# Kernel optimization log

Measured on AMD Instinct MI355X. Metric: run time of the kernel, lower is better.

The kernel has to match this reference:

```python
import jax, jax.numpy as jnp
import numpy as np

V = 30522   # bert-base-uncased vocab size
B, S, D, J, K = 2, 512, 768, 12, 4
NUM_LABELS = 7


def setup_inputs() -> dict:
    key = jax.random.key(0)
    ks = jax.random.split(key, 9)
    return {
        "sequence_output": jax.random.normal(ks[0], (B, S, D), jnp.float32),
        "input_ids": jax.random.randint(ks[1], (B, S), 0, V),
        "neighbors": jax.random.randint(ks[2], (B, S, J, K), 0, V),
        "W_mlp": jax.random.normal(ks[3], (J * D, 13 * D), jnp.float32) * 0.02,
        "b_mlp": jnp.zeros((J * D,), jnp.float32),
        "W_attn": jax.random.normal(ks[4], (D, 2 * D), jnp.float32) * 0.02,
        "b_attn": jnp.zeros((D,), jnp.float32),
        "W_cls": jax.random.normal(ks[5], (NUM_LABELS, 2 * D), jnp.float32) * 0.02,
        "b_cls": jnp.zeros((NUM_LABELS,), jnp.float32),
    }


def _gather_neighbors(sequence_output, input_ids, neighbors):
    """Replicates the dict-based gather-sum. The torch dict persists ACROSS
    batch elements (it is never reset), with later positions overwriting
    earlier ones (last occurrence wins). We carry a [V,D] table + presence
    mask through a scan over the batch dim."""
    pos = jnp.arange(S, dtype=jnp.int32)

    def step(carry, xs):
        table, present = carry            # [V,D], [V] bool
        ids, seq, nb = xs                 # [S], [S,D], [S,J,K]
        # last occurrence index of each vocab id in this example (-1 if absent)
        last_idx = jnp.full((V,), -1, jnp.int32).at[ids].max(pos)
        found = last_idx >= 0
        table = jnp.where(found[:, None],
                          seq[jnp.clip(last_idx, 0, S - 1)], table)
        present = present | found
        # sum neighbor embeddings that are present in the dictionary
        emb = jnp.where(present[nb][..., None], table[nb], 0.0).sum(axis=2)  # [S,J,D]
        return (table, present), emb

    init = (jnp.zeros((V, D), sequence_output.dtype), jnp.zeros((V,), bool))
    _, fn = jax.lax.scan(step, init, (input_ids, sequence_output, neighbors))
    return fn                              # [B,S,J,D]


def reference(sequence_output, input_ids, neighbors,
              W_mlp, b_mlp, W_attn, b_attn, W_cls, b_cls):
    fn = _gather_neighbors(sequence_output, input_ids, neighbors)  # [B,S,J,D]
    n_flat = fn.reshape(B, S, J * D)
    # gated MLP: rij = [row ; neighbors], g = sigmoid(W rij), c' = g * n
    rij = jnp.concatenate([sequence_output, n_flat], axis=-1)      # [B,S,13D]
    g = jax.nn.sigmoid(jnp.einsum('bsf,gf->bsg', rij, W_mlp) + b_mlp)
    c = (g * n_flat).reshape(B, S, J, D)                           # [B,S,J,D]
    # Luong-style attention: query = token embedding, context = gated neighbors
    scores = jnp.einsum('bsd,bsjd->bsj', sequence_output, c)
    attn = jax.nn.softmax(scores, axis=-1)
    mix = jnp.einsum('bsj,bsjd->bsd', attn, c)                     # [B,S,D]
    combined = jnp.concatenate([mix, sequence_output], axis=-1)    # [B,S,2D]
    attn_out = jnp.tanh(jnp.einsum('bsf,df->bsd', combined, W_attn) + b_attn)
    final = jnp.concatenate([sequence_output, attn_out], axis=-1)  # [B,S,2D]
    # dropout is identity at inference
    logits = jnp.einsum('bsf,lf->bsl', final, W_cls) + b_cls       # [B,S,7]
    return logits
```

## Files before the change

kernel.cpp:

```cpp
#include <hip/hip_runtime.h>
#include <hip/hip_bf16.h>

#define V_PAD  30528
#define S_LEN  512
#define D_DIM  768
#define J_N    12
#define M_ROWS 1024
#define K_MLP  9984
#define N_MLP  9216
#define K_ATT  1536
#define N_ATT  768
#define N_LBL  7

using bf16x8 = __attribute__((ext_vector_type(8))) __bf16;
using f32x4  = __attribute__((ext_vector_type(4))) float;

__device__ __forceinline__ unsigned short f2bf(float f) {
  union { float f; unsigned int u; } c; c.f = f;
  unsigned int u = c.u;
  return (unsigned short)((u + 0x7fffu + ((u >> 16) & 1u)) >> 16);
}
__device__ __forceinline__ float bf2f(unsigned short h) {
  union { unsigned int u; float f; } c; c.u = (unsigned int)h << 16; return c.f;
}

__global__ __launch_bounds__(256)
void cvt_bf16_kernel(const float* __restrict__ in, unsigned short* __restrict__ out) {
  size_t i = (size_t)blockIdx.x * 256 + threadIdx.x;
  const float4 f0 = ((const float4*)in)[i * 2];
  const float4 f1 = ((const float4*)in)[i * 2 + 1];
  union { unsigned short h[8]; uint4 q; } pk;
  pk.h[0] = f2bf(f0.x); pk.h[1] = f2bf(f0.y); pk.h[2] = f2bf(f0.z); pk.h[3] = f2bf(f0.w);
  pk.h[4] = f2bf(f1.x); pk.h[5] = f2bf(f1.y); pk.h[6] = f2bf(f1.z); pk.h[7] = f2bf(f1.w);
  ((uint4*)out)[i] = pk.q;
}

__global__ void build_tables_kernel(const int* __restrict__ ids,
                                    int* __restrict__ last0,
                                    int* __restrict__ last01) {
  int p = blockIdx.x * 256 + threadIdx.x;
  if (p < M_ROWS) {
    int id = ids[p];
    atomicMax(&last01[id], p);
    if (p < S_LEN) atomicMax(&last0[id], p);
  }
}

__global__ __launch_bounds__(256) void seqrij_kernel(const float* __restrict__ seq,
                                                     unsigned short* __restrict__ rij) {
  int bs = blockIdx.x;
  for (int d = threadIdx.x; d < D_DIM; d += 256)
    rij[(size_t)bs * K_MLP + d] = f2bf(seq[(size_t)bs * D_DIM + d]);
}

template <bool WRITE_NFLAT>
__global__ __launch_bounds__(192)
void gather_kernel(const float* __restrict__ seq, const int* __restrict__ nbr,
                   const int* __restrict__ last0, const int* __restrict__ last01,
                   float* __restrict__ nflat, unsigned short* __restrict__ rij) {
  const int bsj = blockIdx.x;
  const int j  = bsj % J_N;
  const int bs = bsj / J_N;
  const int b  = bs >> 9;
  const int* nb = nbr + (size_t)bsj * 4;
  const int* tab = (b == 0) ? last0 : last01;
  const int s0 = tab[nb[0]], s1 = tab[nb[1]], s2 = tab[nb[2]], s3 = tab[nb[3]];
  const int d4 = threadIdx.x;
  float4 a = {0.f, 0.f, 0.f, 0.f};
  if (s0 >= 0) { float4 v = ((const float4*)(seq + (size_t)s0 * D_DIM))[d4]; a.x += v.x; a.y += v.y; a.z += v.z; a.w += v.w; }
  if (s1 >= 0) { float4 v = ((const float4*)(seq + (size_t)s1 * D_DIM))[d4]; a.x += v.x; a.y += v.y; a.z += v.z; a.w += v.w; }
  if (s2 >= 0) { float4 v = ((const float4*)(seq + (size_t)s2 * D_DIM))[d4]; a.x += v.x; a.y += v.y; a.z += v.z; a.w += v.w; }
  if (s3 >= 0) { float4 v = ((const float4*)(seq + (size_t)s3 * D_DIM))[d4]; a.x += v.x; a.y += v.y; a.z += v.z; a.w += v.w; }
  union { unsigned short h[4]; unsigned long long q; } pk;
  pk.h[0] = f2bf(a.x); pk.h[1] = f2bf(a.y); pk.h[2] = f2bf(a.z); pk.h[3] = f2bf(a.w);
  *(unsigned long long*)(rij + (size_t)bs * K_MLP + D_DIM + j * D_DIM + d4 * 4) = pk.q;
  if (WRITE_NFLAT)
    ((float4*)(nflat + (size_t)bs * N_MLP + j * D_DIM))[d4] = a;
}

template <int MODE, int TM, int TN, bool BF16B>
__global__ __launch_bounds__(256)
void gemm_nt_kernel(const unsigned short* __restrict__ A,
                    const void* __restrict__ Wv,
                    const float* __restrict__ bias,
                    float* __restrict__ nflat_c,
                    float* __restrict__ outp,
                    int K, int N, int kchunk) {
  constexpr int FM = TM / 32;
  constexpr int FN = TN / 32;
  __shared__ unsigned short ldsA[TM * 32];
  __shared__ unsigned short ldsB[TN * 32];
  const int tid  = threadIdx.x;
  const int lane = tid & 63;
  const int w    = tid >> 6;
  const int m0 = blockIdx.x * TM;
  const int n0 = blockIdx.y * TN;
  const int kb = blockIdx.z * kchunk;

  f32x4 acc[FM][FN];
#pragma unroll
  for (int i = 0; i < FM; ++i)
#pragma unroll
    for (int j = 0; j < FN; ++j) acc[i][j] = (f32x4){0.f, 0.f, 0.f, 0.f};

  const int lr = lane >> 2;
  const int lc = (lane & 3) * 8;
  const int wm = (w >> 1) * (TM / 2), wn = (w & 1) * (TN / 2);
  const int fr = lane & 15;
  const int fk = (lane >> 4) * 8;

  for (int kk = kb; kk < kb + kchunk; kk += 32) {
#pragma unroll
    for (int q = 0; q < TM / 64; ++q) {
      const int r = w * (TM / 4) + q * 16;
      const unsigned short* g = A + (size_t)(m0 + r + lr) * K + kk + lc;
      __builtin_amdgcn_global_load_lds(
          (const __attribute__((address_space(1))) void*)g,
          (__attribute__((address_space(3))) void*)(&ldsA[r * 32]), 16, 0, 0);
    }
    if (BF16B) {
#pragma unroll
      for (int q = 0; q < TN / 64; ++q) {
        const int r = w * (TN / 4) + q * 16;
        const unsigned short* g = (const unsigned short*)Wv +
                                  (size_t)(n0 + r + lr) * K + kk + lc;
        __builtin_amdgcn_global_load_lds(
            (const __attribute__((address_space(1))) void*)g,
            (__attribute__((address_space(3))) void*)(&ldsB[r * 32]), 16, 0, 0);
      }
    } else {
      constexpr int EPT = TN / 8;
      constexpr int TPR = 32 / EPT;
      const int br = tid / TPR, bc = (tid % TPR) * EPT;
      const float* g = (const float*)Wv + (size_t)(n0 + br) * K + kk + bc;
      union { unsigned short h[EPT]; uint4 q[EPT / 8]; } pk;
#pragma unroll
      for (int e = 0; e < EPT; e += 4) {
        float4 f = *(const float4*)(g + e);
        pk.h[e] = f2bf(f.x); pk.h[e + 1] = f2bf(f.y);
        pk.h[e + 2] = f2bf(f.z); pk.h[e + 3] = f2bf(f.w);
      }
      uint4* dst = (uint4*)&ldsB[br * 32 + bc];
#pragma unroll
      for (int e = 0; e < EPT / 8; ++e) dst[e] = pk.q[e];
    }
    __syncthreads();
    bf16x8 aF[FM], bF[FN];
#pragma unroll
    for (int i = 0; i < FM; ++i) aF[i] = *(const bf16x8*)&ldsA[(wm + i * 16 + fr) * 32 + fk];
#pragma unroll
    for (int j = 0; j < FN; ++j) bF[j] = *(const bf16x8*)&ldsB[(wn + j * 16 + fr) * 32 + fk];
#pragma unroll
    for (int i = 0; i < FM; ++i)
#pragma unroll
      for (int j = 0; j < FN; ++j)
        acc[i][j] = __builtin_amdgcn_mfma_f32_16x16x32_bf16(aF[i], bF[j], acc[i][j], 0, 0, 0);
    __syncthreads();
  }

  const size_t zoff = (MODE == 2) ? (size_t)blockIdx.z * M_ROWS * N : 0;
#pragma unroll
  for (int i = 0; i < FM; ++i) {
    int gm0 = m0 + wm + i * 16 + (lane >> 4) * 4;
#pragma unroll
    for (int j = 0; j < FN; ++j) {
      int gn = n0 + wn + j * 16 + (lane & 15);
      float bv = (MODE == 2) ? 0.f : bias[gn];
#pragma unroll
      for (int r = 0; r < 4; ++r) {
        size_t idx = (size_t)(gm0 + r) * N + gn;
        float x = acc[i][j][r] + bv;
        if (MODE == 0) {
          float gg = 1.0f / (1.0f + __expf(-x));
          nflat_c[idx] = gg * nflat_c[idx];
        } else if (MODE == 1) {
          outp[idx] = tanhf(x);
        } else {
          outp[zoff + idx] = x;
        }
      }
    }
  }
}

__global__ __launch_bounds__(256)
void attn_fused_kernel(const float* __restrict__ seq,
                       const float* __restrict__ p0, const float* __restrict__ p1,
                       const float* __restrict__ bmlp,
                       const unsigned short* __restrict__ rij,
                       unsigned short* __restrict__ combined) {
  __shared__ float sc[N_MLP];
  __shared__ float sq[D_DIM];
  __shared__ float ss[J_N];
  const int m = blockIdx.x;
  const int tid = threadIdx.x, lane = tid & 63, w = tid >> 6;
  for (int d = tid; d < D_DIM; d += 256) sq[d] = seq[(size_t)m * D_DIM + d];
  const float* q0 = p0 + (size_t)m * N_MLP;
  const float* q1 = p1 + (size_t)m * N_MLP;
  const unsigned short* nrow = rij + (size_t)m * K_MLP + D_DIM;
  for (int d = tid; d < N_MLP; d += 256) {
    float z = q0[d] + q1[d] + bmlp[d];
    float g = 1.0f / (1.0f + __expf(-z));
    sc[d] = g * bf2f(nrow[d]);
  }
  __syncthreads();
#pragma unroll
  for (int jj = 0; jj < 3; ++jj) {
    int j = w * 3 + jj;
    float p = 0.f;
    for (int d = lane; d < D_DIM; d += 64) p += sq[d] * sc[j * D_DIM + d];
#pragma unroll
    for (int off = 32; off > 0; off >>= 1) p += __shfl_down(p, off);
    if (lane == 0) ss[j] = p;
  }
  __syncthreads();
  float mx = ss[0];
#pragma unroll
  for (int j = 1; j < J_N; ++j) mx = fmaxf(mx, ss[j]);
  float aw[J_N]; float sum = 0.f;
#pragma unroll
  for (int j = 0; j < J_N; ++j) { aw[j] = __expf(ss[j] - mx); sum += aw[j]; }
  float inv = 1.f / sum;
  for (int d = tid; d < D_DIM; d += 256) {
    float mix = 0.f;
#pragma unroll
    for (int j = 0; j < J_N; ++j) mix += aw[j] * sc[j * D_DIM + d];
    combined[(size_t)m * K_ATT + d]         = f2bf(mix * inv);
    combined[(size_t)m * K_ATT + D_DIM + d] = f2bf(sq[d]);
  }
}

__global__ __launch_bounds__(256)
void attn_kernel(const float* __restrict__ seq, const float* __restrict__ c,
                 unsigned short* __restrict__ combined) {
  __shared__ float sc[N_MLP];
  __shared__ float sq[D_DIM];
  __shared__ float ss[J_N];
  const int m = blockIdx.x;
  const int tid = threadIdx.x, lane = tid & 63, w = tid >> 6;
  const float* crow = c + (size_t)m * N_MLP;
  for (int d = tid; d < N_MLP; d += 256) sc[d] = crow[d];
  for (int d = tid; d < D_DIM; d += 256) sq[d] = seq[(size_t)m * D_DIM + d];
  __syncthreads();
#pragma unroll
  for (int jj = 0; jj < 3; ++jj) {
    int j = w * 3 + jj;
    float p = 0.f;
    for (int d = lane; d < D_DIM; d += 64) p += sq[d] * sc[j * D_DIM + d];
#pragma unroll
    for (int off = 32; off > 0; off >>= 1) p += __shfl_down(p, off);
    if (lane == 0) ss[j] = p;
  }
  __syncthreads();
  float mx = ss[0];
#pragma unroll
  for (int j = 1; j < J_N; ++j) mx = fmaxf(mx, ss[j]);
  float aw[J_N]; float sum = 0.f;
#pragma unroll
  for (int j = 0; j < J_N; ++j) { aw[j] = __expf(ss[j] - mx); sum += aw[j]; }
  float inv = 1.f / sum;
  for (int d = tid; d < D_DIM; d += 256) {
    float mix = 0.f;
#pragma unroll
    for (int j = 0; j < J_N; ++j) mix += aw[j] * sc[j * D_DIM + d];
    combined[(size_t)m * K_ATT + d]         = f2bf(mix * inv);
    combined[(size_t)m * K_ATT + D_DIM + d] = f2bf(sq[d]);
  }
}

__global__ __launch_bounds__(256)
void cls_kernel(const float* __restrict__ seq, const float* __restrict__ attnout,
                const float* __restrict__ Wc, const float* __restrict__ bc,
                float* __restrict__ out) {
  __shared__ float part[4][N_LBL];
  const int m = blockIdx.x, tid = threadIdx.x, lane = tid & 63, w = tid >> 6;
  float p[N_LBL] = {0.f, 0.f, 0.f, 0.f, 0.f, 0.f, 0.f};
  for (int f = tid; f < K_ATT; f += 256) {
    float v = (f < D_DIM) ? seq[(size_t)m * D_DIM + f]
                          : attnout[(size_t)m * D_DIM + (f - D_DIM)];
#pragma unroll
    for (int l = 0; l < N_LBL; ++l) p[l] += v * Wc[l * K_ATT + f];
  }
#pragma unroll
  for (int l = 0; l < N_LBL; ++l) {
#pragma unroll
    for (int off = 32; off > 0; off >>= 1) p[l] += __shfl_down(p[l], off);
  }
  if (lane == 0) {
#pragma unroll
    for (int l = 0; l < N_LBL; ++l) part[w][l] = p[l];
  }
  __syncthreads();
  if (tid < N_LBL)
    out[(size_t)m * N_LBL + tid] =
        part[0][tid] + part[1][tid] + part[2][tid] + part[3][tid] + bc[tid];
}

extern "C" void kernel_launch(void* const* d_in, const int* in_sizes, int n_in,
                              void* d_out, int out_size, void* d_ws, size_t ws_size,
                              hipStream_t stream) {
  const float* seq   = (const float*)d_in[0];
  const int*   ids   = (const int*)d_in[1];
  const int*   nbr   = (const int*)d_in[2];
  const float* Wmlp  = (const float*)d_in[3];
  const float* bmlp  = (const float*)d_in[4];
  const float* Wattn = (const float*)d_in[5];
  const float* battn = (const float*)d_in[6];
  const float* Wcls  = (const float*)d_in[7];
  const float* bcls  = (const float*)d_in[8];
  float* out = (float*)d_out;

  char* ws = (char*)d_ws;
  size_t off = 0;
  int* last0  = (int*)(ws + off); off += (size_t)V_PAD * 4;
  int* last01 = (int*)(ws + off); off += (size_t)V_PAD * 4;
  unsigned short* rij = (unsigned short*)(ws + off); off += (size_t)M_ROWS * K_MLP * 2;
  unsigned short* combined = (unsigned short*)(ws + off); off += (size_t)M_ROWS * K_ATT * 2;
  float* attnout = (float*)(ws + off); off += (size_t)M_ROWS * N_ATT * 4;
  const size_t common = off;

  size_t ob = common;
  unsigned short* Wb_mlp  = (unsigned short*)(ws + ob); ob += (size_t)N_MLP * K_MLP * 2;
  unsigned short* Wb_attn = (unsigned short*)(ws + ob); ob += (size_t)N_ATT * K_ATT * 2;
  float* p0 = (float*)(ws + ob); ob += (size_t)M_ROWS * N_MLP * 4;
  float* p1 = (float*)(ws + ob); ob += (size_t)M_ROWS * N_MLP * 4;
  size_t om = common;
  float* nflat_m = (float*)(ws + om); om += (size_t)M_ROWS * N_MLP * 4;
  unsigned short* Wm_mlp  = (unsigned short*)(ws + om); om += (size_t)N_MLP * K_MLP * 2;
  unsigned short* Wm_attn = (unsigned short*)(ws + om); om += (size_t)N_ATT * K_ATT * 2;
  size_t os = common + (size_t)M_ROWS * N_MLP * 4;

  hipMemsetAsync(last0, 0xFF, (size_t)2 * V_PAD * 4, stream);
  build_tables_kernel<<<(M_ROWS + 255) / 256, 256, 0, stream>>>(ids, last0, last01);
  seqrij_kernel<<<M_ROWS, 256, 0, stream>>>(seq, rij);

  if (ws_size >= ob) {
    gather_kernel<false><<<M_ROWS * J_N, 192, 0, stream>>>(seq, nbr, last0, last01, nullptr, rij);
    cvt_bf16_kernel<<<(N_MLP * K_MLP) / (256 * 8), 256, 0, stream>>>(Wmlp, Wb_mlp);
    cvt_bf16_kernel<<<(N_ATT * K_ATT) / (256 * 8), 256, 0, stream>>>(Wattn, Wb_attn);
    gemm_nt_kernel<2, 128, 128, true><<<dim3(M_ROWS / 128, N_MLP / 128, 2), 256, 0, stream>>>(
        rij, Wb_mlp, nullptr, nullptr, p0, K_MLP, N_MLP, K_MLP / 2);
    attn_fused_kernel<<<M_ROWS, 256, 0, stream>>>(seq, p0, p1, bmlp, rij, combined);
    gemm_nt_kernel<1, 64, 64, true><<<dim3(M_ROWS / 64, N_ATT / 64), 256, 0, stream>>>(
        combined, Wb_attn, battn, nullptr, attnout, K_ATT, N_ATT, K_ATT);
  } else if (ws_size >= om) {
    gather_kernel<true><<<M_ROWS * J_N, 192, 0, stream>>>(seq, nbr, last0, last01, nflat_m, rij);
    cvt_bf16_kernel<<<(N_MLP * K_MLP) / (256 * 8), 256, 0, stream>>>(Wmlp, Wm_mlp);
    cvt_bf16_kernel<<<(N_ATT * K_ATT) / (256 * 8), 256, 0, stream>>>(Wattn, Wm_attn);
    gemm_nt_kernel<0, 128, 64, true><<<dim3(M_ROWS / 128, N_MLP / 64), 256, 0, stream>>>(
        rij, Wm_mlp, bmlp, nflat_m, nullptr, K_MLP, N_MLP, K_MLP);
    attn_kernel<<<M_ROWS, 256, 0, stream>>>(seq, nflat_m, combined);
    gemm_nt_kernel<1, 64, 64, true><<<dim3(M_ROWS / 64, N_ATT / 64), 256, 0, stream>>>(
        combined, Wm_attn, battn, nullptr, attnout, K_ATT, N_ATT, K_ATT);
  } else {
    float* nflat_s = nflat_m;
    (void)os;
    gather_kernel<true><<<M_ROWS * J_N, 192, 0, stream>>>(seq, nbr, last0, last01, nflat_s, rij);
    gemm_nt_kernel<0, 128, 64, false><<<dim3(M_ROWS / 128, N_MLP / 64), 256, 0, stream>>>(
        rij, Wmlp, bmlp, nflat_s, nullptr, K_MLP, N_MLP, K_MLP);
    attn_kernel<<<M_ROWS, 256, 0, stream>>>(seq, nflat_s, combined);
    gemm_nt_kernel<1, 64, 64, false><<<dim3(M_ROWS / 64, N_ATT / 64), 256, 0, stream>>>(
        combined, Wattn, battn, nullptr, attnout, K_ATT, N_ATT, K_ATT);
  }
  cls_kernel<<<M_ROWS, 256, 0, stream>>>(seq, attnout, Wcls, bcls, out);
}
```

Measured before the change: 899.7 us.

## Double-buffer GEMM LDS tiles, XOR-swizzle LDS layout, and remap blocks per XCD

The GEMM kernel now uses two LDS buffers, so the next K-slice is staged while MFMAs run on the current one, which also removes one barrier per iteration. LDS columns are XOR-swizzled on both write and read to reduce bank conflicts on the fragment loads. Large GEMMs also remap block IDs so that blocks sharing a weight tile land on the same XCD, aiming for better L2 reuse. In exchange, LDS use doubles, which may lower occupancy for the 128x128 tile, and the swizzle math must match on both the load and read sides.

Measured after the change: 861.0 us. 4.3% less time.

```diff
diff --git a/kernel.cpp b/kernel.cpp
--- a/kernel.cpp
+++ b/kernel.cpp
@@ -78,7 +78,7 @@
     ((float4*)(nflat + (size_t)bs * N_MLP + j * D_DIM))[d4] = a;
 }
 
-template <int MODE, int TM, int TN, bool BF16B>
+template <int MODE, int TM, int TN, bool BF16B, bool SWZ>
 __global__ __launch_bounds__(256)
 void gemm_nt_kernel(const unsigned short* __restrict__ A,
                     const void* __restrict__ Wv,
@@ -88,14 +88,26 @@
                     int K, int N, int kchunk) {
   constexpr int FM = TM / 32;
   constexpr int FN = TN / 32;
-  __shared__ unsigned short ldsA[TM * 32];
-  __shared__ unsigned short ldsB[TN * 32];
+  __shared__ unsigned short ldsA[2][TM * 32];
+  __shared__ unsigned short ldsB[2][TN * 32];
   const int tid  = threadIdx.x;
   const int lane = tid & 63;
   const int w    = tid >> 6;
-  const int m0 = blockIdx.x * TM;
-  const int n0 = blockIdx.y * TN;
-  const int kb = blockIdx.z * kchunk;
+
+  int bx = blockIdx.x, by = blockIdx.y, bz = blockIdx.z;
+  if (SWZ) {
+    const unsigned l   = blockIdx.x + gridDim.x * (blockIdx.y + gridDim.y * blockIdx.z);
+    const unsigned xcd = l & 7u;
+    const unsigned c   = l >> 3;
+    const unsigned gpx = (gridDim.y * gridDim.z) >> 3;
+    const unsigned g   = xcd * gpx + c / gridDim.x;
+    bx = (int)(c % gridDim.x);
+    by = (int)(g % gridDim.y);
+    bz = (int)(g / gridDim.y);
+  }
+  const int m0 = bx * TM;
+  const int n0 = by * TN;
+  const int kb = bz * kchunk;
 
   f32x4 acc[FM][FN];
 #pragma unroll
@@ -103,62 +115,73 @@
 #pragma unroll
     for (int j = 0; j < FN; ++j) acc[i][j] = (f32x4){0.f, 0.f, 0.f, 0.f};
 
-  const int lr = lane >> 2;
-  const int lc = (lane & 3) * 8;
+  const int lr  = lane >> 2;
+  const int lcs = (((lane & 3) ^ ((lane >> 3) & 3)) * 8);
   const int wm = (w >> 1) * (TM / 2), wn = (w & 1) * (TN / 2);
-  const int fr = lane & 15;
-  const int fk = (lane >> 4) * 8;
-
-  for (int kk = kb; kk < kb + kchunk; kk += 32) {
+  const int fr  = lane & 15;
+  const int fc  = (((lane >> 4) ^ ((fr >> 1) & 3)) * 8);
+
+  auto stage = [&](int buf, int kk) {
 #pragma unroll
     for (int q = 0; q < TM / 64; ++q) {
       const int r = w * (TM / 4) + q * 16;
-      const unsigned short* g = A + (size_t)(m0 + r + lr) * K + kk + lc;
+      const unsigned short* gsrc = A + (size_t)(m0 + r + lr) * K + kk + lcs;
       __builtin_amdgcn_global_load_lds(
-          (const __attribute__((address_space(1))) void*)g,
-          (__attribute__((address_space(3))) void*)(&ldsA[r * 32]), 16, 0, 0);
+          (const __attribute__((address_space(1))) void*)gsrc,
+          (__attribute__((address_space(3))) void*)(&ldsA[buf][r * 32]), 16, 0, 0);
     }
     if (BF16B) {
 #pragma unroll
       for (int q = 0; q < TN / 64; ++q) {
         const int r = w * (TN / 4) + q * 16;
-        const unsigned short* g = (const unsigned short*)Wv +
-                                  (size_t)(n0 + r + lr) * K + kk + lc;
+        const unsigned short* gsrc = (const unsigned short*)Wv +
+                                     (size_t)(n0 + r + lr) * K + kk + lcs;
         __builtin_amdgcn_global_load_lds(
-            (const __attribute__((address_space(1))) void*)g,
-            (__attribute__((address_space(3))) void*)(&ldsB[r * 32]), 16, 0, 0);
+            (const __attribute__((address_space(1))) void*)gsrc,
+            (__attribute__((address_space(3))) void*)(&ldsB[buf][r * 32]), 16, 0, 0);
       }
     } else {
       constexpr int EPT = TN / 8;
       constexpr int TPR = 32 / EPT;
       const int br = tid / TPR, bc = (tid % TPR) * EPT;
-      const float* g = (const float*)Wv + (size_t)(n0 + br) * K + kk + bc;
-      union { unsigned short h[EPT]; uint4 q[EPT / 8]; } pk;
-#pragma unroll
-      for (int e = 0; e < EPT; e += 4) {
-        float4 f = *(const float4*)(g + e);
-        pk.h[e] = f2bf(f.x); pk.h[e + 1] = f2bf(f.y);
-        pk.h[e + 2] = f2bf(f.z); pk.h[e + 3] = f2bf(f.w);
+      const float* gsrc = (const float*)Wv + (size_t)(n0 + br) * K + kk + bc;
+      const int brs = (br >> 1) & 3;
+#pragma unroll
+      for (int e = 0; e < EPT; e += 8) {
+        union { unsigned short h[8]; uint4 q4; } pk;
+#pragma unroll
+        for (int e2 = 0; e2 < 8; e2 += 4) {
+          float4 f = *(const float4*)(gsrc + e + e2);
+          pk.h[e2]     = f2bf(f.x); pk.h[e2 + 1] = f2bf(f.y);
+          pk.h[e2 + 2] = f2bf(f.z); pk.h[e2 + 3] = f2bf(f.w);
+        }
+        const int slot = ((bc + e) >> 3) ^ brs;
+        *(uint4*)&ldsB[buf][br * 32 + slot * 8] = pk.q4;
       }
-      uint4* dst = (uint4*)&ldsB[br * 32 + bc];
-#pragma unroll
-      for (int e = 0; e < EPT / 8; ++e) dst[e] = pk.q[e];
     }
+  };
+
+  const int nt = kchunk >> 5;
+  stage(0, kb);
+  for (int t = 0; t < nt; ++t) {
+    const int cur = t & 1;
     __syncthreads();
+    if (t + 1 < nt) stage(cur ^ 1, kb + (t + 1) * 32);
     bf16x8 aF[FM], bF[FN];
 #pragma unroll
-    for (int i = 0; i < FM; ++i) aF[i] = *(const bf16x8*)&ldsA[(wm + i * 16 + fr) * 32 + fk];
-#pragma unroll
-    for (int j = 0; j < FN; ++j) bF[j] = *(const bf16x8*)&ldsB[(wn + j * 16 + fr) * 32 + fk];
+    for (int i = 0; i < FM; ++i)
+      aF[i] = *(const bf16x8*)&ldsA[cur][(wm + i * 16 + fr) * 32 + fc];
+#pragma unroll
+    for (int j = 0; j < FN; ++j)
+      bF[j] = *(const bf16x8*)&ldsB[cur][(wn + j * 16 + fr) * 32 + fc];
 #pragma unroll
     for (int i = 0; i < FM; ++i)
 #pragma unroll
       for (int j = 0; j < FN; ++j)
         acc[i][j] = __builtin_amdgcn_mfma_f32_16x16x32_bf16(aF[i], bF[j], acc[i][j], 0, 0, 0);
-    __syncthreads();
-  }
-
-  const size_t zoff = (MODE == 2) ? (size_t)blockIdx.z * M_ROWS * N : 0;
+  }
+
+  const size_t zoff = (MODE == 2) ? (size_t)bz * M_ROWS * N : 0;
 #pragma unroll
   for (int i = 0; i < FM; ++i) {
     int gm0 = m0 + wm + i * 16 + (lane >> 4) * 4;
@@ -338,28 +361,28 @@
     gather_kernel<false><<<M_ROWS * J_N, 192, 0, stream>>>(seq, nbr, last0, last01, nullptr, rij);
     cvt_bf16_kernel<<<(N_MLP * K_MLP) / (256 * 8), 256, 0, stream>>>(Wmlp, Wb_mlp);
     cvt_bf16_kernel<<<(N_ATT * K_ATT) / (256 * 8), 256, 0, stream>>>(Wattn, Wb_attn);
-    gemm_nt_kernel<2, 128, 128, true><<<dim3(M_ROWS / 128, N_MLP / 128, 2), 256, 0, stream>>>(
+    gemm_nt_kernel<2, 128, 128, true, true><<<dim3(M_ROWS / 128, N_MLP / 128, 2), 256, 0, stream>>>(
         rij, Wb_mlp, nullptr, nullptr, p0, K_MLP, N_MLP, K_MLP / 2);
     attn_fused_kernel<<<M_ROWS, 256, 0, stream>>>(seq, p0, p1, bmlp, rij, combined);
-    gemm_nt_kernel<1, 64, 64, true><<<dim3(M_ROWS / 64, N_ATT / 64), 256, 0, stream>>>(
+    gemm_nt_kernel<1, 64, 64, true, false><<<dim3(M_ROWS / 64, N_ATT / 64), 256, 0, stream>>>(
         combined, Wb_attn, battn, nullptr, attnout, K_ATT, N_ATT, K_ATT);
   } else if (ws_size >= om) {
     gather_kernel<true><<<M_ROWS * J_N, 192, 0, stream>>>(seq, nbr, last0, last01, nflat_m, rij);
     cvt_bf16_kernel<<<(N_MLP * K_MLP) / (256 * 8), 256, 0, stream>>>(Wmlp, Wm_mlp);
     cvt_bf16_kernel<<<(N_ATT * K_ATT) / (256 * 8), 256, 0, stream>>>(Wattn, Wm_attn);
-    gemm_nt_kernel<0, 128, 64, true><<<dim3(M_ROWS / 128, N_MLP / 64), 256, 0, stream>>>(
+    gemm_nt_kernel<0, 128, 64, true, true><<<dim3(M_ROWS / 128, N_MLP / 64), 256, 0, stream>>>(
         rij, Wm_mlp, bmlp, nflat_m, nullptr, K_MLP, N_MLP, K_MLP);
     attn_kernel<<<M_ROWS, 256, 0, stream>>>(seq, nflat_m, combined);
-    gemm_nt_kernel<1, 64, 64, true><<<dim3(M_ROWS / 64, N_ATT / 64), 256, 0, stream>>>(
+    gemm_nt_kernel<1, 64, 64, true, false><<<dim3(M_ROWS / 64, N_ATT / 64), 256, 0, stream>>>(
         combined, Wm_attn, battn, nullptr, attnout, K_ATT, N_ATT, K_ATT);
   } else {
     float* nflat_s = nflat_m;
     (void)os;
     gather_kernel<true><<<M_ROWS * J_N, 192, 0, stream>>>(seq, nbr, last0, last01, nflat_s, rij);
-    gemm_nt_kernel<0, 128, 64, false><<<dim3(M_ROWS / 128, N_MLP / 64), 256, 0, stream>>>(
+    gemm_nt_kernel<0, 128, 64, false, true><<<dim3(M_ROWS / 128, N_MLP / 64), 256, 0, stream>>>(
         rij, Wmlp, bmlp, nflat_s, nullptr, K_MLP, N_MLP, K_MLP);
     attn_kernel<<<M_ROWS, 256, 0, stream>>>(seq, nflat_s, combined);
-    gemm_nt_kernel<1, 64, 64, false><<<dim3(M_ROWS / 64, N_ATT / 64), 256, 0, stream>>>(
+    gemm_nt_kernel<1, 64, 64, false, false><<<dim3(M_ROWS / 64, N_ATT / 64), 256, 0, stream>>>(
         combined, Wattn, battn, nullptr, attnout, K_ATT, N_ATT, K_ATT);
   }
   cls_kernel<<<M_ROWS, 256, 0, stream>>>(seq, attnout, Wcls, bcls, out);
```
